# Optimization experiments

Measured on AMD Instinct MI355X. Metric: run time of the kernel, lower is better.

Reference implementation:

```python
import jax, jax.numpy as jnp
import numpy as np
import math

N_HEADS = 8
TANH_CLIP = 10.0
TEMP = 1.0


def setup_inputs() -> dict:
    key = jax.random.key(0)
    ks = jax.random.split(key, 8)
    B, N, D = 256, 2048, 128
    node_embeddings = jax.random.normal(ks[0], (B, N, D), dtype=jnp.float32)
    W_node = jax.random.normal(ks[1], (D, 3 * D), dtype=jnp.float32) / math.sqrt(D)
    W_fixed = jax.random.normal(ks[2], (D, D), dtype=jnp.float32) / math.sqrt(D)
    W_step = jax.random.normal(ks[3], (2 * D, D), dtype=jnp.float32) / math.sqrt(2 * D)
    W_out = jax.random.normal(ks[4], (D, D), dtype=jnp.float32) / math.sqrt(D)
    first_idx = jax.random.randint(ks[5], (B,), 0, N, dtype=jnp.int32)
    last_idx = jax.random.randint(ks[6], (B,), 0, N, dtype=jnp.int32)
    mask = jax.random.bernoulli(ks[7], 0.5, (B, N))
    mask = mask.at[:, 0].set(False)  # guarantee at least one feasible node per row
    return {"node_embeddings": node_embeddings, "W_node": W_node, "W_fixed": W_fixed,
            "W_step": W_step, "W_out": W_out, "first_idx": first_idx,
            "last_idx": last_idx, "mask": mask}


def reference(node_embeddings, W_node, W_fixed, W_step, W_out, first_idx, last_idx, mask):
    B, N, D = node_embeddings.shape
    H = N_HEADS
    hd = D // H  # key_dim = val_dim = embed_dim / n_heads
    neg_inf = -jnp.inf

    # --- _precompute ---
    graph_embed = node_embeddings.mean(axis=1)                # [B, D]
    fixed_context = graph_embed @ W_fixed                     # [B, D]
    proj = node_embeddings @ W_node                           # [B, N, 3D]
    gK, gV, logit_K = jnp.split(proj, 3, axis=-1)             # each [B, N, D]
    gK = gK.reshape(B, N, H, hd).transpose(2, 0, 1, 3)        # [H, B, N, hd]
    gV = gV.reshape(B, N, H, hd).transpose(2, 0, 1, 3)        # [H, B, N, hd]

    # --- step context: cat(first node emb, last node emb) ---
    first_emb = jnp.take_along_axis(node_embeddings, first_idx[:, None, None].astype(jnp.int32), axis=1)[:, 0]  # [B, D]
    last_emb = jnp.take_along_axis(node_embeddings, last_idx[:, None, None].astype(jnp.int32), axis=1)[:, 0]
    step_ctx = jnp.concatenate([first_emb, last_emb], axis=-1)  # [B, 2D]
    query = fixed_context + step_ctx @ W_step                 # [B, D]

    # --- glimpse multi-head attention (n_query = 1, masked inner) ---
    Q = query.reshape(B, H, hd).transpose(1, 0, 2)            # [H, B, hd]
    compat = jnp.einsum('hbd,hbnd->hbn', Q, gK) / math.sqrt(hd)  # [H, B, N]
    compat = jnp.where(mask[None, :, :], neg_inf, compat)     # mask_inner=True
    attn = jax.nn.softmax(compat, axis=-1)
    heads = jnp.einsum('hbn,hbnd->hbd', attn, gV)             # [H, B, hd]
    glimpse = heads.transpose(1, 0, 2).reshape(B, D) @ W_out  # project_out, [B, D]

    # --- logits with tanh clipping and masking ---
    logits = jnp.einsum('bd,bnd->bn', glimpse, logit_K) / math.sqrt(D)  # [B, N]
    logits = jnp.tanh(logits) * TANH_CLIP
    logits = jnp.where(mask, neg_inf, logits)                 # mask_logits=True
    log_p = jax.nn.log_softmax(logits / TEMP, axis=-1)        # [B, N]
    return log_p
```

## Files before the change

### kernel.cpp

```cpp
#include <hip/hip_runtime.h>
#include <math.h>

#define B_ 256
#define N_ 2048
#define D_ 128

#define NEG_HUGE (-1.0e30f)

#define WSA_STRIDE 1040
#define WSA_SIZE (B_ * 8 * WSA_STRIDE)
#define WSB_OFF WSA_SIZE
#define WSB_SIZE (B_ * 8 * 2)
#define WSC_OFF (WSB_OFF + WSB_SIZE)

typedef __attribute__((ext_vector_type(8))) short bf16x8;
typedef __attribute__((ext_vector_type(4))) float f32x4;
typedef __attribute__((ext_vector_type(4))) unsigned short u16x4;
typedef __attribute__((ext_vector_type(2))) int i32x2;

__device__ __forceinline__ float wave_max64(float v) {
#pragma unroll
  for (int off = 32; off > 0; off >>= 1) v = fmaxf(v, __shfl_xor(v, off, 64));
  return v;
}
__device__ __forceinline__ float wave_sum64(float v) {
#pragma unroll
  for (int off = 32; off > 0; off >>= 1) v += __shfl_xor(v, off, 64);
  return v;
}
__device__ __forceinline__ unsigned short bf16rne(float f) {
  unsigned u = __float_as_uint(f);
  u += 0x7FFFu + ((u >> 16) & 1u);
  return (unsigned short)(u >> 16);
}

__global__ void __launch_bounds__(128) k_partial(const float* __restrict__ emb,
                                                 float* __restrict__ buf) {
  const int b = blockIdx.x, s = blockIdx.y;
  const int t = threadIdx.x;
  const int f4 = t & 31, ng = t >> 5;
  const float4* base = (const float4*)(emb + (size_t)b * N_ * D_);
  float4 acc = make_float4(0.f, 0.f, 0.f, 0.f);
  int n = s * 256 + ng;
#pragma unroll 4
  for (int i = 0; i < 64; ++i, n += 4) {
    float4 v = base[(size_t)n * 32 + f4];
    acc.x += v.x; acc.y += v.y; acc.z += v.z; acc.w += v.w;
  }
  __shared__ float4 red[128];
  red[t] = acc;
  __syncthreads();
  if (ng == 0) {
    float4 a = red[f4], bb = red[32 + f4], c = red[64 + f4], d = red[96 + f4];
    float4 r = make_float4(a.x + bb.x + c.x + d.x, a.y + bb.y + c.y + d.y,
                           a.z + bb.z + c.z + d.z, a.w + bb.w + c.w + d.w);
    *((float4*)(buf + (size_t)b * N_ + s * 128) + f4) = r;
  }
}

__global__ void __launch_bounds__(128) k_query(const float* __restrict__ emb,
                                               const float* __restrict__ Wfix,
                                               const float* __restrict__ Wstep,
                                               const float* __restrict__ Wnode,
                                               const int* __restrict__ fidx,
                                               const int* __restrict__ lidx,
                                               float* __restrict__ buf) {
  const int b = blockIdx.x, t = threadIdx.x;
  __shared__ float ge[128], fe[128], le[128], q[128];
  float s = 0.f;
  const float* part = buf + (size_t)b * N_;
#pragma unroll
  for (int i = 0; i < 8; ++i) s += part[i * 128 + t];
  ge[t] = s * (1.0f / 2048.0f);
  const int fi = fidx[b], li = lidx[b];
  fe[t] = emb[(size_t)b * N_ * D_ + (size_t)fi * D_ + t];
  le[t] = emb[(size_t)b * N_ * D_ + (size_t)li * D_ + t];
  __syncthreads();
  float acc = 0.f;
  for (int k = 0; k < 128; ++k) acc = fmaf(ge[k], Wfix[k * 128 + t], acc);
  for (int k = 0; k < 128; ++k) acc = fmaf(fe[k], Wstep[k * 128 + t], acc);
  for (int k = 0; k < 128; ++k) acc = fmaf(le[k], Wstep[(128 + k) * 128 + t], acc);
  q[t] = acc;
  __syncthreads();
  const float* wrow = Wnode + (size_t)t * 384;
#pragma unroll
  for (int h = 0; h < 8; ++h) {
    float a = 0.f;
#pragma unroll
    for (int k = 0; k < 16; ++k) a = fmaf(q[h * 16 + k], wrow[h * 16 + k], a);
    buf[(size_t)b * N_ + 1024 + h * 128 + t] = a * 0.25f;
  }
}

__global__ void __launch_bounds__(256) k_attn_m(const float* __restrict__ emb,
                                                const unsigned char* __restrict__ mask,
                                                const float* __restrict__ buf,
                                                float* __restrict__ wsA) {
  const int b = blockIdx.x, s = blockIdx.y, t = threadIdx.x;
  const int lane = t & 63, w = t >> 6;
  const int lg = lane >> 4, lc = lane & 15;

  __shared__ __align__(16) unsigned short eR[9216];
  __shared__ __align__(16) unsigned short pT[16 * 72];
  __shared__ float red0[4][16];
  __shared__ float red1[4][16];
  __shared__ float resc_s[16];
  __shared__ unsigned char mask_s[64];

  bf16x8 bq[4];
#pragma unroll
  for (int ks = 0; ks < 4; ++ks)
#pragma unroll
    for (int j = 0; j < 8; ++j) bq[ks][j] = 0;
  if (lc < 8) {
    const float* qrow = buf + (size_t)b * N_ + 1024 + lc * 128;
#pragma unroll
    for (int ks = 0; ks < 4; ++ks)
#pragma unroll
      for (int j = 0; j < 8; ++j)
        bq[ks][j] = (short)bf16rne(qrow[32 * ks + 8 * lg + j]);
  }

  float m_run = -INFINITY, l_run = 0.f;
  f32x4 wacc0 = {0.f, 0.f, 0.f, 0.f}, wacc1 = {0.f, 0.f, 0.f, 0.f};
  const float* embb = emb + ((size_t)b * N_ + s * 256) * D_;
  const unsigned char* mrow = mask + (size_t)b * N_ + s * 256;

  for (int tile = 0; tile < 4; ++tile) {
    {
      const float* src = embb + (size_t)tile * 64 * D_;
#pragma unroll
      for (int i = 0; i < 4; ++i) {
        const int gid = t + 256 * i;
        const int n = gid >> 4, d0 = (gid & 15) * 8;
        const float4 v0 = *(const float4*)(src + (size_t)n * D_ + d0);
        const float4 v1 = *(const float4*)(src + (size_t)n * D_ + d0 + 4);
        bf16x8 ev;
        ev[0] = (short)bf16rne(v0.x); ev[1] = (short)bf16rne(v0.y);
        ev[2] = (short)bf16rne(v0.z); ev[3] = (short)bf16rne(v0.w);
        ev[4] = (short)bf16rne(v1.x); ev[5] = (short)bf16rne(v1.y);
        ev[6] = (short)bf16rne(v1.z); ev[7] = (short)bf16rne(v1.w);
        const int widx = ((n >> 2) * 8 + (d0 >> 4)) * 72 + ((n & 3) << 4) + (d0 & 15);
        *(bf16x8*)&eR[widx] = ev;
      }
      if (t < 64) mask_s[t] = mrow[tile * 64 + t];
    }
    __syncthreads();

    f32x4 sAcc = {0.f, 0.f, 0.f, 0.f};
#pragma unroll
    for (int ks = 0; ks < 4; ++ks) {
      const int aidx = ((4 * w + (lc >> 2)) * 8 + 2 * ks + (lg >> 1)) * 72 +
                       ((lc & 3) << 4) + ((lg & 1) << 3);
      const bf16x8 af = *(const bf16x8*)&eR[aidx];
      sAcc = __builtin_amdgcn_mfma_f32_16x16x32_bf16(af, bq[ks], sAcc, 0, 0, 0);
    }

    float sv[4];
    bool mk[4];
    float tmax = -INFINITY;
#pragma unroll
    for (int r = 0; r < 4; ++r) {
      mk[r] = mask_s[16 * w + 4 * lg + r] != 0;
      sv[r] = mk[r] ? -INFINITY : sAcc[r];
      tmax = fmaxf(tmax, sv[r]);
    }
    tmax = fmaxf(tmax, __shfl_xor(tmax, 16, 64));
    tmax = fmaxf(tmax, __shfl_xor(tmax, 32, 64));
    if (lane < 16) red0[w][lc] = tmax;
    __syncthreads();

    const float m_tile = fmaxf(fmaxf(red0[0][lc], red0[1][lc]),
                               fmaxf(red0[2][lc], red0[3][lc]));
    const float m_new = fmaxf(m_run, m_tile);
    const float rsc = (m_new == -INFINITY) ? 1.f : __expf(m_run - m_new);
    float psum = 0.f;
    unsigned short pu[4];
#pragma unroll
    for (int r = 0; r < 4; ++r) {
      const float p = mk[r] ? 0.f : __expf(sv[r] - m_new);
      psum += p;
      pu[r] = bf16rne(p);
    }
    m_run = m_new;
    psum += __shfl_xor(psum, 16, 64);
    psum += __shfl_xor(psum, 32, 64);
    if (lane < 16) red1[w][lc] = psum;
    *(u16x4*)&pT[lc * 72 + 16 * w + 4 * lg] = (u16x4){pu[0], pu[1], pu[2], pu[3]};
    if (t < 16) resc_s[t] = rsc;
    __syncthreads();

    l_run = l_run * rsc + (red1[0][lc] + red1[1][lc] + red1[2][lc] + red1[3][lc]);

    {
      const float r0f = resc_s[4 * lg + 0], r1f = resc_s[4 * lg + 1];
      const float r2f = resc_s[4 * lg + 2], r3f = resc_s[4 * lg + 3];
      wacc0[0] *= r0f; wacc0[1] *= r1f; wacc0[2] *= r2f; wacc0[3] *= r3f;
      wacc1[0] *= r0f; wacc1[1] *= r1f; wacc1[2] *= r2f; wacc1[3] *= r3f;
    }

    i32x2 tb0a, tb0b, tb1a, tb1b, tb2a, tb2b, tb3a, tb3b;
    {
      const unsigned base00 = (unsigned)(unsigned long long)
          &eR[((0 + 2 * lg) * 8 + w) * 72 + lc];
      const unsigned base01 = (unsigned)(unsigned long long)
          &eR[((0 + 2 * lg) * 8 + (w + 4)) * 72 + lc];
      const unsigned base10 = (unsigned)(unsigned long long)
          &eR[((8 + 2 * lg) * 8 + w) * 72 + lc];
      const unsigned base11 = (unsigned)(unsigned long long)
          &eR[((8 + 2 * lg) * 8 + (w + 4)) * 72 + lc];
      asm volatile("ds_read_b64_tr_b16 %0, %2 offset:0\n\t"
                   "ds_read_b64_tr_b16 %1, %2 offset:1152"
                   : "=v"(tb0a), "=v"(tb0b) : "v"(base00));
      asm volatile("ds_read_b64_tr_b16 %0, %2 offset:0\n\t"
                   "ds_read_b64_tr_b16 %1, %2 offset:1152"
                   : "=v"(tb1a), "=v"(tb1b) : "v"(base01));
      asm volatile("ds_read_b64_tr_b16 %0, %2 offset:0\n\t"
                   "ds_read_b64_tr_b16 %1, %2 offset:1152"
                   : "=v"(tb2a), "=v"(tb2b) : "v"(base10));
      asm volatile("ds_read_b64_tr_b16 %0, %2 offset:0\n\t"
                   "ds_read_b64_tr_b16 %1, %2 offset:1152"
                   : "=v"(tb3a), "=v"(tb3b) : "v"(base11));
      asm volatile("s_waitcnt lgkmcnt(0)" ::: "memory");
      __builtin_amdgcn_sched_barrier(0);
    }
    {
      const bf16x8 pa0 = *(const bf16x8*)&pT[lc * 72 + 8 * lg];
      const bf16x8 pa1 = *(const bf16x8*)&pT[lc * 72 + 32 + 8 * lg];
      union { i32x2 d[2]; bf16x8 v; } u;
      u.d[0] = tb0a; u.d[1] = tb0b;
      wacc0 = __builtin_amdgcn_mfma_f32_16x16x32_bf16(pa0, u.v, wacc0, 0, 0, 0);
      u.d[0] = tb1a; u.d[1] = tb1b;
      wacc1 = __builtin_amdgcn_mfma_f32_16x16x32_bf16(pa0, u.v, wacc1, 0, 0, 0);
      u.d[0] = tb2a; u.d[1] = tb2b;
      wacc0 = __builtin_amdgcn_mfma_f32_16x16x32_bf16(pa1, u.v, wacc0, 0, 0, 0);
      u.d[0] = tb3a; u.d[1] = tb3b;
      wacc1 = __builtin_amdgcn_mfma_f32_16x16x32_bf16(pa1, u.v, wacc1, 0, 0, 0);
    }
    __syncthreads();
  }

  float* dst = wsA + (size_t)(b * 8 + s) * WSA_STRIDE;
  if (lg < 2) {
#pragma unroll
    for (int r = 0; r < 4; ++r) {
      const int h = 4 * lg + r;
      dst[16 + h * 128 + 16 * w + lc] = wacc0[r];
      dst[16 + h * 128 + 16 * (w + 4) + lc] = wacc1[r];
    }
  }
  if (t < 8) { dst[t] = m_run; dst[8 + t] = l_run; }
}

__global__ void __launch_bounds__(128) k_attn_comb(const float* __restrict__ Wnode,
                                                   const float* __restrict__ Wout,
                                                   const float* __restrict__ wsA,
                                                   float* __restrict__ wsC) {
  const int b = blockIdx.x, t = threadIdx.x;
  const float* base = wsA + (size_t)b * 8 * WSA_STRIDE;
  __shared__ float Ls[8], scale[8][8];
  __shared__ float wl[8 * 128], heads[128], glim[128];

  if (t < 8) {
    float M = -INFINITY;
#pragma unroll
    for (int s = 0; s < 8; ++s) M = fmaxf(M, base[s * WSA_STRIDE + t]);
    float L = 0.f;
#pragma unroll
    for (int s = 0; s < 8; ++s) {
      const float m = base[s * WSA_STRIDE + t];
      const float sc = (m == -INFINITY) ? 0.f : expf(m - M);
      scale[s][t] = sc;
      L = fmaf(base[s * WSA_STRIDE + 8 + t], sc, L);
    }
    Ls[t] = L;
  }
  __syncthreads();
#pragma unroll
  for (int h = 0; h < 8; ++h) {
    float acc = 0.f;
#pragma unroll
    for (int s = 0; s < 8; ++s)
      acc = fmaf(scale[s][h], base[s * WSA_STRIDE + 16 + h * 128 + t], acc);
    wl[h * 128 + t] = acc;
  }
  __syncthreads();
  {
    const int h = t >> 4, k = t & 15;
    float hv = 0.f;
    const float* wp = Wnode + 128 + h * 16 + k;
    for (int d = 0; d < 128; ++d) hv = fmaf(wl[h * 128 + d], wp[(size_t)d * 384], hv);
    heads[t] = hv / Ls[h];
  }
  __syncthreads();
  {
    float g = 0.f;
    for (int j = 0; j < 128; ++j) g = fmaf(heads[j], Wout[j * 128 + t], g);
    glim[t] = g;
  }
  __syncthreads();
  {
    float cv = 0.f;
    const float* wr = Wnode + (size_t)t * 384 + 256;
    for (int j = 0; j < 128; ++j) cv = fmaf(wr[j], glim[j], cv);
    wsC[(size_t)b * 128 + t] = cv * 0.08838834764831845f;
  }
}

__global__ void __launch_bounds__(256) k_logits_part(const float* __restrict__ emb,
                                                     const unsigned char* __restrict__ mask,
                                                     const float* __restrict__ wsC,
                                                     float* __restrict__ buf,
                                                     float* __restrict__ wsB) {
  const int b = blockIdx.x, s = blockIdx.y;
  const int t = threadIdx.x, lane = t & 63, w = t >> 6;
  __shared__ float lg[64];
  const float4 cf = ((const float4*)(wsC + (size_t)b * 128))[t & 31];
  const float* embb = emb + ((size_t)b * N_ + s * 256) * D_;
  const unsigned char* mrow = mask + (size_t)b * N_ + s * 256;
  float mr = NEG_HUGE, sr = 0.f;

  for (int tile = 0; tile < 4; ++tile) {
    const int n0 = tile * 64;
#pragma unroll
    for (int i = 0; i < 8; ++i) {
      const int gid = t + 256 * i;
      const int r = gid >> 5, c = (gid & 31) * 4;
      const float4 e = *(const float4*)(embb + (size_t)(n0 + r) * D_ + c);
      float p = fmaf(e.x, cf.x, fmaf(e.y, cf.y, fmaf(e.z, cf.z, e.w * cf.w)));
      p += __shfl_xor(p, 16, 64);
      p += __shfl_xor(p, 8, 64);
      p += __shfl_xor(p, 4, 64);
      p += __shfl_xor(p, 2, 64);
      p += __shfl_xor(p, 1, 64);
      if ((t & 31) == 0) lg[r] = p;
    }
    __syncthreads();

    const bool mk = mrow[n0 + lane] != 0;
    const float x = lg[lane];
    const float ex = __expf(2.f * x);
    const float val = mk ? NEG_HUGE : (10.f - __fdividef(20.f, ex + 1.f));
    const float tm = wave_max64(val);
    const float mn = fmaxf(mr, tm);
    sr = sr * __expf(mr - mn) + wave_sum64(mk ? 0.f : __expf(val - mn));
    mr = mn;
    if (w == 0) buf[(size_t)b * N_ + s * 256 + n0 + lane] = val;
    __syncthreads();
  }
  if (t == 0) {
    wsB[(size_t)(b * 8 + s) * 2] = mr;
    wsB[(size_t)(b * 8 + s) * 2 + 1] = sr;
  }
}

__global__ void __launch_bounds__(256) k_norm(const float* __restrict__ wsB,
                                              float* __restrict__ buf) {
  const int b = blockIdx.x, t = threadIdx.x;
  __shared__ float LSs;
  if (t == 0) {
    float M = NEG_HUGE;
#pragma unroll
    for (int q = 0; q < 8; ++q) M = fmaxf(M, wsB[(size_t)(b * 8 + q) * 2]);
    float S = 0.f;
#pragma unroll
    for (int q = 0; q < 8; ++q) {
      const float m = wsB[(size_t)(b * 8 + q) * 2];
      S += wsB[(size_t)(b * 8 + q) * 2 + 1] * expf(m - M);
    }
    LSs = M + logf(S);
  }
  __syncthreads();
  const float LS = LSs;
#pragma unroll
  for (int i = 0; i < 8; ++i) {
    const size_t idx = (size_t)b * N_ + t + 256 * i;
    const float v = buf[idx];
    buf[idx] = (v <= -1.0e29f) ? NEG_HUGE : (v - LS);
  }
}

extern "C" void kernel_launch(void* const* d_in, const int* in_sizes, int n_in,
                              void* d_out, int out_size, void* d_ws, size_t ws_size,
                              hipStream_t stream) {
  (void)in_sizes; (void)n_in; (void)out_size; (void)ws_size;
  const float* emb = (const float*)d_in[0];
  const float* Wnode = (const float*)d_in[1];
  const float* Wfix = (const float*)d_in[2];
  const float* Wstep = (const float*)d_in[3];
  const float* Wout = (const float*)d_in[4];
  const int* fidx = (const int*)d_in[5];
  const int* lidx = (const int*)d_in[6];
  const unsigned char* mask = (const unsigned char*)d_in[7];
  float* buf = (float*)d_out;
  float* ws = (float*)d_ws;

  k_partial<<<dim3(B_, 8), 128, 0, stream>>>(emb, buf);
  k_query<<<B_, 128, 0, stream>>>(emb, Wfix, Wstep, Wnode, fidx, lidx, buf);
  k_attn_m<<<dim3(B_, 8), 256, 0, stream>>>(emb, mask, buf, ws);
  k_attn_comb<<<B_, 128, 0, stream>>>(Wnode, Wout, ws, ws + WSC_OFF);
  k_logits_part<<<dim3(B_, 8), 256, 0, stream>>>(emb, mask, ws + WSC_OFF, buf, ws + WSB_OFF);
  k_norm<<<B_, 256, 0, stream>>>(ws + WSB_OFF, buf);
}
```

Before: 167.6 us.

## Materialize a bf16 copy of embeddings in workspace for later passes

The mean-reduction pass now also writes a bf16 copy of the node embeddings into the workspace. The attention and logit passes then read that half-size copy instead of re-reading and converting the fp32 tensor. This cuts total HBM traffic over the three passes over the embeddings. In exchange it adds a 128 MB write, and the logit dot products now use bf16 inputs, which lowers their precision. A fallback path keeps the old fp32 behaviour when the workspace is too small.

```diff
diff --git a/kernel.cpp b/kernel.cpp
--- a/kernel.cpp
+++ b/kernel.cpp
@@ -7,11 +7,15 @@
 
 #define NEG_HUGE (-1.0e30f)
 
+#define WSE_USHORTS ((size_t)B_ * N_ * D_)
+#define WSE_BYTES (WSE_USHORTS * 2)
 #define WSA_STRIDE 1040
 #define WSA_SIZE (B_ * 8 * WSA_STRIDE)
 #define WSB_OFF WSA_SIZE
 #define WSB_SIZE (B_ * 8 * 2)
 #define WSC_OFF (WSB_OFF + WSB_SIZE)
+#define WS_TAIL_FLOATS (WSC_OFF + B_ * D_)
+#define WS_NEED_BYTES (WSE_BYTES + (size_t)WS_TAIL_FLOATS * 4)
 
 typedef __attribute__((ext_vector_type(8))) short bf16x8;
 typedef __attribute__((ext_vector_type(4))) float f32x4;
@@ -33,28 +37,39 @@
   u += 0x7FFFu + ((u >> 16) & 1u);
   return (unsigned short)(u >> 16);
 }
-
-__global__ void __launch_bounds__(128) k_partial(const float* __restrict__ emb,
-                                                 float* __restrict__ buf) {
-  const int b = blockIdx.x, s = blockIdx.y;
-  const int t = threadIdx.x;
-  const int f4 = t & 31, ng = t >> 5;
-  const float4* base = (const float4*)(emb + (size_t)b * N_ * D_);
+__device__ __forceinline__ float bflo(unsigned u) { return __uint_as_float(u << 16); }
+__device__ __forceinline__ float bfhi(unsigned u) { return __uint_as_float(u & 0xFFFF0000u); }
+
+template <bool SH>
+__global__ void __launch_bounds__(256) k_prep(const float* __restrict__ emb,
+                                              unsigned short* __restrict__ wsE,
+                                              float* __restrict__ buf) {
+  const int b = blockIdx.x, s = blockIdx.y, t = threadIdx.x;
+  const int f4 = t & 31, g = t >> 5;
+  const size_t rowbase = (size_t)b * N_;
   float4 acc = make_float4(0.f, 0.f, 0.f, 0.f);
-  int n = s * 256 + ng;
+  int n = s * 256 + g;
 #pragma unroll 4
-  for (int i = 0; i < 64; ++i, n += 4) {
-    float4 v = base[(size_t)n * 32 + f4];
+  for (int i = 0; i < 32; ++i, n += 8) {
+    const float4 v = *(const float4*)(emb + (rowbase + n) * D_ + f4 * 4);
     acc.x += v.x; acc.y += v.y; acc.z += v.z; acc.w += v.w;
-  }
-  __shared__ float4 red[128];
+    if (SH) {
+      ushort4 o;
+      o.x = bf16rne(v.x); o.y = bf16rne(v.y); o.z = bf16rne(v.z); o.w = bf16rne(v.w);
+      *(ushort4*)(wsE + (rowbase + n) * D_ + f4 * 4) = o;
+    }
+  }
+  __shared__ float4 red[256];
   red[t] = acc;
   __syncthreads();
-  if (ng == 0) {
-    float4 a = red[f4], bb = red[32 + f4], c = red[64 + f4], d = red[96 + f4];
-    float4 r = make_float4(a.x + bb.x + c.x + d.x, a.y + bb.y + c.y + d.y,
-                           a.z + bb.z + c.z + d.z, a.w + bb.w + c.w + d.w);
-    *((float4*)(buf + (size_t)b * N_ + s * 128) + f4) = r;
+  if (g == 0) {
+    float4 r = red[f4];
+#pragma unroll
+    for (int j = 1; j < 8; ++j) {
+      const float4 a = red[j * 32 + f4];
+      r.x += a.x; r.y += a.y; r.z += a.z; r.w += a.w;
+    }
+    *(float4*)(buf + (size_t)b * N_ + s * 128 + f4 * 4) = r;
   }
 }
 
@@ -92,7 +107,9 @@
   }
 }
 
+template <bool SH>
 __global__ void __launch_bounds__(256) k_attn_m(const float* __restrict__ emb,
+                                                const unsigned short* __restrict__ wsE,
                                                 const unsigned char* __restrict__ mask,
                                                 const float* __restrict__ buf,
                                                 float* __restrict__ wsA) {
@@ -124,24 +141,30 @@
   float m_run = -INFINITY, l_run = 0.f;
   f32x4 wacc0 = {0.f, 0.f, 0.f, 0.f}, wacc1 = {0.f, 0.f, 0.f, 0.f};
   const float* embb = emb + ((size_t)b * N_ + s * 256) * D_;
+  const unsigned short* embB = wsE + ((size_t)b * N_ + s * 256) * D_;
   const unsigned char* mrow = mask + (size_t)b * N_ + s * 256;
 
   for (int tile = 0; tile < 4; ++tile) {
     {
-      const float* src = embb + (size_t)tile * 64 * D_;
 #pragma unroll
       for (int i = 0; i < 4; ++i) {
         const int gid = t + 256 * i;
         const int n = gid >> 4, d0 = (gid & 15) * 8;
-        const float4 v0 = *(const float4*)(src + (size_t)n * D_ + d0);
-        const float4 v1 = *(const float4*)(src + (size_t)n * D_ + d0 + 4);
-        bf16x8 ev;
-        ev[0] = (short)bf16rne(v0.x); ev[1] = (short)bf16rne(v0.y);
-        ev[2] = (short)bf16rne(v0.z); ev[3] = (short)bf16rne(v0.w);
-        ev[4] = (short)bf16rne(v1.x); ev[5] = (short)bf16rne(v1.y);
-        ev[6] = (short)bf16rne(v1.z); ev[7] = (short)bf16rne(v1.w);
         const int widx = ((n >> 2) * 8 + (d0 >> 4)) * 72 + ((n & 3) << 4) + (d0 & 15);
-        *(bf16x8*)&eR[widx] = ev;
+        if (SH) {
+          const uint4 u = *(const uint4*)(embB + ((size_t)tile * 64 + n) * D_ + d0);
+          *(uint4*)&eR[widx] = u;
+        } else {
+          const float* src = embb + (size_t)tile * 64 * D_;
+          const float4 v0 = *(const float4*)(src + (size_t)n * D_ + d0);
+          const float4 v1 = *(const float4*)(src + (size_t)n * D_ + d0 + 4);
+          bf16x8 ev;
+          ev[0] = (short)bf16rne(v0.x); ev[1] = (short)bf16rne(v0.y);
+          ev[2] = (short)bf16rne(v0.z); ev[3] = (short)bf16rne(v0.w);
+          ev[4] = (short)bf16rne(v1.x); ev[5] = (short)bf16rne(v1.y);
+          ev[6] = (short)bf16rne(v1.z); ev[7] = (short)bf16rne(v1.w);
+          *(bf16x8*)&eR[widx] = ev;
+        }
       }
       if (t < 64) mask_s[t] = mrow[tile * 64 + t];
     }
@@ -307,7 +330,9 @@
   }
 }
 
+template <bool SH>
 __global__ void __launch_bounds__(256) k_logits_part(const float* __restrict__ emb,
+                                                     const unsigned short* __restrict__ wsE,
                                                      const unsigned char* __restrict__ mask,
                                                      const float* __restrict__ wsC,
                                                      float* __restrict__ buf,
@@ -315,25 +340,53 @@
   const int b = blockIdx.x, s = blockIdx.y;
   const int t = threadIdx.x, lane = t & 63, w = t >> 6;
   __shared__ float lg[64];
-  const float4 cf = ((const float4*)(wsC + (size_t)b * 128))[t & 31];
   const float* embb = emb + ((size_t)b * N_ + s * 256) * D_;
+  const unsigned short* embB = wsE + ((size_t)b * N_ + s * 256) * D_;
   const unsigned char* mrow = mask + (size_t)b * N_ + s * 256;
   float mr = NEG_HUGE, sr = 0.f;
 
+  float4 cfa, cfb;
+  float4 cf4;
+  if (SH) {
+    const float4* c4 = (const float4*)(wsC + (size_t)b * 128);
+    cfa = c4[(t & 15) * 2];
+    cfb = c4[(t & 15) * 2 + 1];
+  } else {
+    cf4 = ((const float4*)(wsC + (size_t)b * 128))[t & 31];
+  }
+
   for (int tile = 0; tile < 4; ++tile) {
     const int n0 = tile * 64;
-#pragma unroll
-    for (int i = 0; i < 8; ++i) {
-      const int gid = t + 256 * i;
-      const int r = gid >> 5, c = (gid & 31) * 4;
-      const float4 e = *(const float4*)(embb + (size_t)(n0 + r) * D_ + c);
-      float p = fmaf(e.x, cf.x, fmaf(e.y, cf.y, fmaf(e.z, cf.z, e.w * cf.w)));
-      p += __shfl_xor(p, 16, 64);
-      p += __shfl_xor(p, 8, 64);
-      p += __shfl_xor(p, 4, 64);
-      p += __shfl_xor(p, 2, 64);
-      p += __shfl_xor(p, 1, 64);
-      if ((t & 31) == 0) lg[r] = p;
+    if (SH) {
+#pragma unroll
+      for (int i = 0; i < 4; ++i) {
+        const int gid = t + 256 * i;
+        const int r = gid >> 4, c8 = (gid & 15) * 8;
+        const uint4 u = *(const uint4*)(embB + (size_t)(n0 + r) * D_ + c8);
+        float p = bflo(u.x) * cfa.x + bfhi(u.x) * cfa.y;
+        p = fmaf(bflo(u.y), cfa.z, p); p = fmaf(bfhi(u.y), cfa.w, p);
+        p = fmaf(bflo(u.z), cfb.x, p); p = fmaf(bfhi(u.z), cfb.y, p);
+        p = fmaf(bflo(u.w), cfb.z, p); p = fmaf(bfhi(u.w), cfb.w, p);
+        p += __shfl_xor(p, 8, 64);
+        p += __shfl_xor(p, 4, 64);
+        p += __shfl_xor(p, 2, 64);
+        p += __shfl_xor(p, 1, 64);
+        if ((t & 15) == 0) lg[r] = p;
+      }
+    } else {
+#pragma unroll
+      for (int i = 0; i < 8; ++i) {
+        const int gid = t + 256 * i;
+        const int r = gid >> 5, c = (gid & 31) * 4;
+        const float4 e = *(const float4*)(embb + (size_t)(n0 + r) * D_ + c);
+        float p = fmaf(e.x, cf4.x, fmaf(e.y, cf4.y, fmaf(e.z, cf4.z, e.w * cf4.w)));
+        p += __shfl_xor(p, 16, 64);
+        p += __shfl_xor(p, 8, 64);
+        p += __shfl_xor(p, 4, 64);
+        p += __shfl_xor(p, 2, 64);
+        p += __shfl_xor(p, 1, 64);
+        if ((t & 31) == 0) lg[r] = p;
+      }
     }
     __syncthreads();
 
@@ -383,7 +436,7 @@
 extern "C" void kernel_launch(void* const* d_in, const int* in_sizes, int n_in,
                               void* d_out, int out_size, void* d_ws, size_t ws_size,
                               hipStream_t stream) {
-  (void)in_sizes; (void)n_in; (void)out_size; (void)ws_size;
+  (void)in_sizes; (void)n_in; (void)out_size;
   const float* emb = (const float*)d_in[0];
   const float* Wnode = (const float*)d_in[1];
   const float* Wfix = (const float*)d_in[2];
@@ -393,12 +446,26 @@
   const int* lidx = (const int*)d_in[6];
   const unsigned char* mask = (const unsigned char*)d_in[7];
   float* buf = (float*)d_out;
-  float* ws = (float*)d_ws;
-
-  k_partial<<<dim3(B_, 8), 128, 0, stream>>>(emb, buf);
-  k_query<<<B_, 128, 0, stream>>>(emb, Wfix, Wstep, Wnode, fidx, lidx, buf);
-  k_attn_m<<<dim3(B_, 8), 256, 0, stream>>>(emb, mask, buf, ws);
-  k_attn_comb<<<B_, 128, 0, stream>>>(Wnode, Wout, ws, ws + WSC_OFF);
-  k_logits_part<<<dim3(B_, 8), 256, 0, stream>>>(emb, mask, ws + WSC_OFF, buf, ws + WSB_OFF);
-  k_norm<<<B_, 256, 0, stream>>>(ws + WSB_OFF, buf);
-}
+
+  if (ws_size >= WS_NEED_BYTES) {
+    unsigned short* wsE = (unsigned short*)d_ws;
+    float* fb = (float*)((char*)d_ws + WSE_BYTES);
+    k_prep<true><<<dim3(B_, 8), 256, 0, stream>>>(emb, wsE, buf);
+    k_query<<<B_, 128, 0, stream>>>(emb, Wfix, Wstep, Wnode, fidx, lidx, buf);
+    k_attn_m<true><<<dim3(B_, 8), 256, 0, stream>>>(emb, wsE, mask, buf, fb);
+    k_attn_comb<<<B_, 128, 0, stream>>>(Wnode, Wout, fb, fb + WSC_OFF);
+    k_logits_part<true><<<dim3(B_, 8), 256, 0, stream>>>(emb, wsE, mask, fb + WSC_OFF,
+                                                         buf, fb + WSB_OFF);
+    k_norm<<<B_, 256, 0, stream>>>(fb + WSB_OFF, buf);
+  } else {
+    float* fb = (float*)d_ws;
+    unsigned short* wsE = (unsigned short*)d_ws;
+    k_prep<false><<<dim3(B_, 8), 256, 0, stream>>>(emb, wsE, buf);
+    k_query<<<B_, 128, 0, stream>>>(emb, Wfix, Wstep, Wnode, fidx, lidx, buf);
+    k_attn_m<false><<<dim3(B_, 8), 256, 0, stream>>>(emb, wsE, mask, buf, fb);
+    k_attn_comb<<<B_, 128, 0, stream>>>(Wnode, Wout, fb, fb + WSC_OFF);
+    k_logits_part<false><<<dim3(B_, 8), 256, 0, stream>>>(emb, wsE, mask, fb + WSC_OFF,
+                                                          buf, fb + WSB_OFF);
+    k_norm<<<B_, 256, 0, stream>>>(fb + WSB_OFF, buf);
+  }
+}
```

Result: no change. 166.3 us (-0.8%).
